# Optimization experiments

Measured on AMD Instinct MI355X. Metric: run time of the kernel, lower is better.

Reference implementation:

```python
import jax, jax.numpy as jnp
import numpy as np

LN_EPS = 1e-5

def setup_inputs() -> dict:
    key = jax.random.key(0)
    ks = jax.random.split(key, 8)
    B, L, D, H = 4, 2048, 512, 8
    x = jax.random.normal(ks[0], (B, L, D), dtype=jnp.float32)
    token_ids = jax.random.randint(ks[1], (B, L), 0, 50000, dtype=jnp.int64)
    s = 1.0 / np.sqrt(D)
    Wq = jax.random.normal(ks[2], (D, D), dtype=jnp.float32) * s
    Wk = jax.random.normal(ks[3], (D, D), dtype=jnp.float32) * s
    Wv = jax.random.normal(ks[4], (D, D), dtype=jnp.float32) * s
    Wo = jax.random.normal(ks[5], (D, D), dtype=jnp.float32) * s
    gamma = jnp.ones((D,), dtype=jnp.float32)
    beta = jnp.zeros((D,), dtype=jnp.float32)
    return {"x": x, "token_ids": token_ids, "Wq": Wq, "Wk": Wk,
            "Wv": Wv, "Wo": Wo, "gamma": gamma, "beta": beta}

def reference(x, token_ids, Wq, Wk, Wv, Wo, gamma, beta):
    B, L, D = x.shape
    H = 8
    Dh = D // H
    residual = x
    # Pre-LN
    mu = jnp.mean(x, axis=-1, keepdims=True)
    var = jnp.mean(jnp.square(x - mu), axis=-1, keepdims=True)
    xn = (x - mu) * jax.lax.rsqrt(var + LN_EPS) * gamma + beta
    # projections (torch Linear: y = x @ W.T), split heads -> [B,H,L,Dh]
    def proj(W):
        return jnp.einsum('bld,ed->ble', xn, W).reshape(B, L, H, Dh).transpose(0, 2, 1, 3)
    Q, K, V = proj(Wq), proj(Wk), proj(Wv)
    scale = jnp.sqrt(jnp.float32(Dh))
    scores = jnp.einsum('bhqd,bhkd->bhqk', Q, K) / scale  # [B,H,L,L]
    neg_inf = jnp.float32(-jnp.inf)
    causal = jnp.triu(jnp.ones((L, L), dtype=bool), k=1)           # [L,L]
    pad = (token_ids == 0)[:, None, None, :]                       # [B,1,1,L]
    scores = jnp.where(causal[None, None], neg_inf, scores)
    scores = jnp.where(pad, neg_inf, scores)
    all_masked = jnp.all(jnp.isinf(scores), axis=-1, keepdims=True)
    scores = jnp.where(all_masked, 0.0, scores)
    attn = jax.nn.softmax(scores, axis=-1)  # dropout is identity in eval
    out = jnp.einsum('bhqk,bhkd->bhqd', attn, V)
    out = out.transpose(0, 2, 1, 3).reshape(B, L, D)
    out = jnp.einsum('bld,ed->ble', out, Wo)
    return residual + out
```

## Files before the change

### kernel.cpp

```cpp
#include <hip/hip_runtime.h>
#include <math.h>

typedef unsigned short u16;
typedef unsigned int u32;
typedef unsigned long long u64;
typedef float f32x4 __attribute__((ext_vector_type(4)));
typedef __bf16 bf16x8 __attribute__((ext_vector_type(8)));
typedef __bf16 bf16x4 __attribute__((ext_vector_type(4)));

constexpr int Bc = 4, Lc = 2048, Dc = 512, Hc = 8, DHc = 64;
constexpr int NTOK = Bc * Lc;
constexpr float LN_EPS = 1e-5f;
constexpr int KS = 72;
constexpr int PS = 72;
constexpr float QSCALE = 0.125f * 1.44269504088896340736f;

__device__ inline u16 bf_bits(float f) {
  return __builtin_bit_cast(u16, (__bf16)f);
}

__global__ __launch_bounds__(256) void cvt4_kernel(const float* __restrict__ s0,
                                                   const float* __restrict__ s1,
                                                   const float* __restrict__ s2,
                                                   const float* __restrict__ s3,
                                                   u16* __restrict__ d0,
                                                   u16* __restrict__ d1,
                                                   u16* __restrict__ d2,
                                                   u16* __restrict__ d3) {
  int mat = blockIdx.x >> 8;
  int i = ((blockIdx.x & 255) * 256 + threadIdx.x) * 4;
  const float* s = (mat == 0) ? s0 : (mat == 1) ? s1 : (mat == 2) ? s2 : s3;
  u16* d = (mat == 0) ? d0 : (mat == 1) ? d1 : (mat == 2) ? d2 : d3;
  float4 v = *(const float4*)&s[i];
  bf16x4 o;
  o[0] = (__bf16)v.x; o[1] = (__bf16)v.y; o[2] = (__bf16)v.z; o[3] = (__bf16)v.w;
  *(bf16x4*)&d[i] = o;
}

__global__ __launch_bounds__(256) void pmask_kernel(const int* __restrict__ tok,
                                                    u64* __restrict__ pm) {
  int wid = (blockIdx.x * 256 + threadIdx.x) >> 6;
  int lane = threadIdx.x & 63;
  u64 m = __ballot(tok[(size_t)wid * 64 + lane] == 0);
  if (lane == 0) pm[wid] = m;
}

__global__ __launch_bounds__(256) void ln_kernel(const float* __restrict__ x,
                                                 const float* __restrict__ gamma,
                                                 const float* __restrict__ beta,
                                                 u16* __restrict__ xn) {
  int wave = threadIdx.x >> 6;
  int lane = threadIdx.x & 63;
  int row  = blockIdx.x * 4 + wave;
  const float* xr = x + (size_t)row * Dc;
  float4 v0 = ((const float4*)xr)[lane * 2];
  float4 v1 = ((const float4*)xr)[lane * 2 + 1];
  float sum = v0.x + v0.y + v0.z + v0.w + v1.x + v1.y + v1.z + v1.w;
  float sq  = v0.x*v0.x + v0.y*v0.y + v0.z*v0.z + v0.w*v0.w
            + v1.x*v1.x + v1.y*v1.y + v1.z*v1.z + v1.w*v1.w;
  #pragma unroll
  for (int off = 32; off > 0; off >>= 1) {
    sum += __shfl_xor(sum, off);
    sq  += __shfl_xor(sq, off);
  }
  float mu = sum * (1.0f / Dc);
  float rs = rsqrtf(sq * (1.0f / Dc) - mu * mu + LN_EPS);
  float4 g0 = ((const float4*)gamma)[lane * 2];
  float4 g1 = ((const float4*)gamma)[lane * 2 + 1];
  float4 b0 = ((const float4*)beta)[lane * 2];
  float4 b1 = ((const float4*)beta)[lane * 2 + 1];
  bf16x8 o;
  o[0] = (__bf16)((v0.x - mu) * rs * g0.x + b0.x);
  o[1] = (__bf16)((v0.y - mu) * rs * g0.y + b0.y);
  o[2] = (__bf16)((v0.z - mu) * rs * g0.z + b0.z);
  o[3] = (__bf16)((v0.w - mu) * rs * g0.w + b0.w);
  o[4] = (__bf16)((v1.x - mu) * rs * g1.x + b1.x);
  o[5] = (__bf16)((v1.y - mu) * rs * g1.y + b1.y);
  o[6] = (__bf16)((v1.z - mu) * rs * g1.z + b1.z);
  o[7] = (__bf16)((v1.w - mu) * rs * g1.w + b1.w);
  *(bf16x8*)&xn[(size_t)row * Dc + lane * 8] = o;
}

template <int MODE>
__global__ __launch_bounds__(256) void gemm_bf16(const u16* __restrict__ A,
                                                 const u16* __restrict__ W,
                                                 const float* __restrict__ res,
                                                 float* __restrict__ out_f,
                                                 u16* __restrict__ o_q,
                                                 u16* __restrict__ o_k,
                                                 u16* __restrict__ o_v,
                                                 float* __restrict__ vm) {
  __shared__ u16 As[128 * KS];
  __shared__ u16 Bs[128 * KS];
  int tid = threadIdx.x;
  int lane = tid & 63;
  int w = tid >> 6;
  int wr = w >> 1, wc = w & 1;
  int cc = lane & 15, rb = lane >> 4;
  int n0 = blockIdx.x * 128;
  int e0 = blockIdx.y * 128;
  f32x4 acc[4][4] = {};
  for (int k0 = 0; k0 < Dc; k0 += 64) {
    #pragma unroll
    for (int u = 0; u < 4; u++) {
      int idx = u * 256 + tid;
      int row = idx >> 3;
      int col = (idx & 7) << 3;
      *(uint4*)&As[row * KS + col] = *(const uint4*)&A[(size_t)(n0 + row) * Dc + k0 + col];
      *(uint4*)&Bs[row * KS + col] = *(const uint4*)&W[(size_t)(e0 + row) * Dc + k0 + col];
    }
    __syncthreads();
    #pragma unroll
    for (int kk = 0; kk < 64; kk += 32) {
      bf16x8 aF[4], bF[4];
      #pragma unroll
      for (int m = 0; m < 4; m++)
        aF[m] = *(bf16x8*)&As[(wr * 64 + m * 16 + cc) * KS + kk + rb * 8];
      #pragma unroll
      for (int n = 0; n < 4; n++)
        bF[n] = *(bf16x8*)&Bs[(wc * 64 + n * 16 + cc) * KS + kk + rb * 8];
      #pragma unroll
      for (int m = 0; m < 4; m++)
        #pragma unroll
        for (int n = 0; n < 4; n++)
          acc[m][n] = __builtin_amdgcn_mfma_f32_16x16x32_bf16(aF[m], bF[n], acc[m][n], 0, 0, 0);
    }
    __syncthreads();
  }
  if (MODE == 3) {
    int bb = n0 >> 11;
    #pragma unroll
    for (int n = 0; n < 4; n++) {
      int c = e0 + wc * 64 + n * 16 + cc;
      int mat = c >> 9;
      int cm = c & 511;
      int h = cm >> 6, dh = cm & 63;
      if (mat == 2) {
        float cp = 0.f;
        #pragma unroll
        for (int m = 0; m < 4; m++) {
          int l0 = (n0 + wr * 64 + m * 16 + rb * 4) & (Lc - 1);
          bf16x4 o4;
          o4[0] = (__bf16)acc[m][n][0]; o4[1] = (__bf16)acc[m][n][1];
          o4[2] = (__bf16)acc[m][n][2]; o4[3] = (__bf16)acc[m][n][3];
          *(bf16x4*)&o_v[((size_t)(bb * Hc + h) * DHc + dh) * Lc + l0] = o4;
          cp += (acc[m][n][0] + acc[m][n][1]) + (acc[m][n][2] + acc[m][n][3]);
        }
        cp += __shfl_xor(cp, 16);
        cp += __shfl_xor(cp, 32);
        if (lane < 16) atomicAdd(&vm[(bb * Hc + h) * DHc + dh], cp);
      } else {
        u16* dst = (mat == 0) ? o_q : o_k;
        float sc = (mat == 0) ? QSCALE : 1.0f;
        #pragma unroll
        for (int m = 0; m < 4; m++) {
          #pragma unroll
          for (int j = 0; j < 4; j++) {
            int r = n0 + wr * 64 + m * 16 + rb * 4 + j;
            int ll = r & (Lc - 1);
            dst[(((size_t)(bb * Hc + h)) * Lc + ll) * DHc + dh] = bf_bits(acc[m][n][j] * sc);
          }
        }
      }
    }
  } else {
    #pragma unroll
    for (int m = 0; m < 4; m++) {
      #pragma unroll
      for (int n = 0; n < 4; n++) {
        #pragma unroll
        for (int j = 0; j < 4; j++) {
          int r = n0 + wr * 64 + m * 16 + rb * 4 + j;
          int c = e0 + wc * 64 + n * 16 + cc;
          size_t o = (size_t)r * Dc + c;
          out_f[o] = acc[m][n][j] + res[o];
        }
      }
    }
  }
}

__global__ __launch_bounds__(64) void attn3(const u16* __restrict__ Q,
                                            const u16* __restrict__ K,
                                            const u16* __restrict__ VT,
                                            const float* __restrict__ vm,
                                            const u64* __restrict__ pmask,
                                            u16* __restrict__ out) {
  __shared__ u16 Ps[32 * PS];
  int lane = threadIdx.x;
  int cc = lane & 15, rb = lane >> 4;
  int bh = blockIdx.x;
  int qt = (int)gridDim.y - 1 - (int)blockIdx.y;
  int q0 = qt * 32;
  int b = bh >> 3, h = bh & 7;
  const u16* Qb = Q + (size_t)bh * Lc * DHc;
  const u16* Kb = K + (size_t)bh * Lc * DHc;
  const u16* Vb = VT + (size_t)bh * DHc * Lc;
  const u64* pmb = pmask + (b << 5);

  bf16x8 qF[2][2];
  #pragma unroll
  for (int qb = 0; qb < 2; qb++)
    #pragma unroll
    for (int kc = 0; kc < 2; kc++)
      qF[qb][kc] = *(const bf16x8*)&Qb[(size_t)(q0 + qb * 16 + cc) * DHc + kc * 32 + rb * 8];

  float mrow[2] = {-INFINITY, -INFINITY};
  float lrow[2] = {0.f, 0.f};
  f32x4 acc[2][4] = {};
  int nfull = q0 >> 6;

  bf16x8 kf[4][2];
  #pragma unroll
  for (int c = 0; c < 4; c++) {
    const u16* kp = &Kb[(size_t)(c * 16 + cc) * DHc + rb * 8];
    kf[c][0] = *(const bf16x8*)kp;
    kf[c][1] = *(const bf16x8*)(kp + 32);
  }

  for (int kt = 0; kt <= nfull; kt++) {
    int k0 = kt * 64;
    bool last = (kt == nfull);
    u64 pm = pmb[kt];
    bf16x8 vf[2][4];
    #pragma unroll
    for (int kc = 0; kc < 2; kc++)
      #pragma unroll
      for (int d0 = 0; d0 < 4; d0++)
        vf[kc][d0] = *(const bf16x8*)&Vb[(size_t)(d0 * 16 + cc) * Lc + k0 + kc * 32 + rb * 8];

    f32x4 sq[2][4] = {};
    __builtin_amdgcn_s_setprio(1);
    #pragma unroll
    for (int c = 0; c < 4; c++) {
      #pragma unroll
      for (int qb = 0; qb < 2; qb++) {
        sq[qb][c] = __builtin_amdgcn_mfma_f32_16x16x32_bf16(kf[c][0], qF[qb][0], sq[qb][c], 0, 0, 0);
        sq[qb][c] = __builtin_amdgcn_mfma_f32_16x16x32_bf16(kf[c][1], qF[qb][1], sq[qb][c], 0, 0, 0);
      }
    }
    __builtin_amdgcn_s_setprio(0);
    if (!last) {
      #pragma unroll
      for (int c = 0; c < 4; c++) {
        const u16* kp = &Kb[(size_t)(k0 + 64 + c * 16 + cc) * DHc + rb * 8];
        kf[c][0] = *(const bf16x8*)kp;
        kf[c][1] = *(const bf16x8*)(kp + 32);
      }
    }
    #pragma unroll
    for (int c = 0; c < 4; c++) {
      u32 smr = (((u32)(pm >> (c * 16)) & 0xffffu) >> (rb * 4));
      #pragma unroll
      for (int qb = 0; qb < 2; qb++)
        #pragma unroll
        for (int j = 0; j < 4; j++)
          if ((smr >> j) & 1) sq[qb][c][j] = -INFINITY;
    }
    if (last) {
      #pragma unroll
      for (int qb = 0; qb < 2; qb++) {
        int qrel = q0 + qb * 16 + cc - k0;
        #pragma unroll
        for (int c = 0; c < 4; c++)
          #pragma unroll
          for (int j = 0; j < 4; j++)
            if (c * 16 + rb * 4 + j > qrel) sq[qb][c][j] = -INFINITY;
      }
    }
    #pragma unroll
    for (int qb = 0; qb < 2; qb++) {
      float m0 = fmaxf(fmaxf(sq[qb][0][0], sq[qb][0][1]), fmaxf(sq[qb][0][2], sq[qb][0][3]));
      float m1 = fmaxf(fmaxf(sq[qb][1][0], sq[qb][1][1]), fmaxf(sq[qb][1][2], sq[qb][1][3]));
      float m2 = fmaxf(fmaxf(sq[qb][2][0], sq[qb][2][1]), fmaxf(sq[qb][2][2], sq[qb][2][3]));
      float m3 = fmaxf(fmaxf(sq[qb][3][0], sq[qb][3][1]), fmaxf(sq[qb][3][2], sq[qb][3][3]));
      float mx = fmaxf(fmaxf(m0, m1), fmaxf(m2, m3));
      mx = fmaxf(mx, __shfl_xor(mx, 16));
      mx = fmaxf(mx, __shfl_xor(mx, 32));
      if (!__all(mx <= mrow[qb] + 8.f)) {
        float nm = fmaxf(mrow[qb], mx);
        float nm2 = fmaxf(nm, -1e30f);
        float alpha = exp2f(mrow[qb] - nm2);
        lrow[qb] *= alpha;
        #pragma unroll
        for (int d0 = 0; d0 < 4; d0++)
          #pragma unroll
          for (int j = 0; j < 4; j++)
            acc[qb][d0][j] *= alpha;
        mrow[qb] = nm;
      }
      float nm2 = fmaxf(mrow[qb], -1e30f);
      float rs = 0.f;
      #pragma unroll
      for (int c = 0; c < 4; c++) {
        f32x4 p;
        #pragma unroll
        for (int j = 0; j < 4; j++) p[j] = exp2f(sq[qb][c][j] - nm2);
        rs += (p[0] + p[1]) + (p[2] + p[3]);
        bf16x4 p4;
        p4[0] = (__bf16)p[0]; p4[1] = (__bf16)p[1];
        p4[2] = (__bf16)p[2]; p4[3] = (__bf16)p[3];
        *(bf16x4*)&Ps[(qb * 16 + cc) * PS + c * 16 + rb * 4] = p4;
      }
      rs += __shfl_xor(rs, 16);
      rs += __shfl_xor(rs, 32);
      lrow[qb] += rs;
    }
    asm volatile("s_waitcnt lgkmcnt(0)" ::: "memory");
    __builtin_amdgcn_sched_barrier(0);
    __builtin_amdgcn_s_setprio(1);
    #pragma unroll
    for (int kc = 0; kc < 2; kc++) {
      bf16x8 pF0 = *(bf16x8*)&Ps[(size_t)cc * PS + kc * 32 + rb * 8];
      bf16x8 pF1 = *(bf16x8*)&Ps[(size_t)(16 + cc) * PS + kc * 32 + rb * 8];
      #pragma unroll
      for (int d0 = 0; d0 < 4; d0++) {
        acc[0][d0] = __builtin_amdgcn_mfma_f32_16x16x32_bf16(vf[kc][d0], pF0, acc[0][d0], 0, 0, 0);
        acc[1][d0] = __builtin_amdgcn_mfma_f32_16x16x32_bf16(vf[kc][d0], pF1, acc[1][d0], 0, 0, 0);
      }
    }
    __builtin_amdgcn_s_setprio(0);
  }
  #pragma unroll
  for (int qb = 0; qb < 2; qb++) {
    int q = q0 + qb * 16 + cc;
    bool ok = lrow[qb] > 0.f;
    float inv = ok ? 1.0f / lrow[qb] : 0.f;
    #pragma unroll
    for (int d0 = 0; d0 < 4; d0++) {
      bf16x4 o4;
      #pragma unroll
      for (int j = 0; j < 4; j++) {
        float v = ok ? acc[qb][d0][j] * inv
                     : vm[bh * DHc + d0 * 16 + rb * 4 + j] * (1.0f / Lc);
        o4[j] = (__bf16)v;
      }
      *(bf16x4*)&out[((size_t)(b * Lc + q)) * Dc + h * DHc + d0 * 16 + rb * 4] = o4;
    }
  }
}

extern "C" void kernel_launch(void* const* d_in, const int* in_sizes, int n_in,
                              void* d_out, int out_size, void* d_ws, size_t ws_size,
                              hipStream_t stream) {
  const float* x     = (const float*)d_in[0];
  const int*   tok   = (const int*)d_in[1];
  const float* Wq    = (const float*)d_in[2];
  const float* Wk    = (const float*)d_in[3];
  const float* Wv    = (const float*)d_in[4];
  const float* Wo    = (const float*)d_in[5];
  const float* gamma = (const float*)d_in[6];
  const float* beta  = (const float*)d_in[7];
  float* out = (float*)d_out;

  const size_t SEG = (size_t)NTOK * Dc;
  const size_t WSEG = (size_t)Dc * Dc;
  u16* xn   = (u16*)d_ws;
  u16* Qd   = xn + SEG;
  u16* Kd   = Qd + SEG;
  u16* VT   = Kd + SEG;
  u16* ao   = VT + SEG;
  u16* Wqkv = ao + SEG;
  u16* Wob  = Wqkv + 3 * WSEG;
  float* vm = (float*)(Wob + WSEG);
  u64* pmarr = (u64*)(vm + (size_t)Bc * Hc * DHc);

  (void)hipMemsetAsync(vm, 0, (size_t)Bc * Hc * DHc * sizeof(float), stream);

  cvt4_kernel<<<1024, 256, 0, stream>>>(Wq, Wk, Wv, Wo,
                                        Wqkv, Wqkv + WSEG, Wqkv + 2 * WSEG, Wob);
  ln_kernel<<<NTOK / 4, 256, 0, stream>>>(x, gamma, beta, xn);
  pmask_kernel<<<32, 256, 0, stream>>>(tok, pmarr);

  dim3 gq(NTOK / 128, (3 * Dc) / 128);
  gemm_bf16<3><<<gq, 256, 0, stream>>>(xn, Wqkv, nullptr, nullptr, Qd, Kd, VT, vm);

  dim3 ga(Bc * Hc, Lc / 32);
  attn3<<<ga, 64, 0, stream>>>(Qd, Kd, VT, vm, pmarr, ao);

  dim3 gg(NTOK / 128, Dc / 128);
  gemm_bf16<0><<<gg, 256, 0, stream>>>(ao, Wob, x, out, nullptr, nullptr, nullptr, nullptr);
}
```

Measured before the change: 123.5 us.

## Split attention KV loop across two waves, stage GEMM epilogues through LDS, retile V

The attention kernel now runs two waves per block, each handling alternate 64-key tiles, and merges their online-softmax states through shared memory at the end. It also skips padding-mask application when a tile holds no padded tokens. V is stored in 64-token tiles so each tile is contiguous, and the QKV and output GEMM epilogues go through LDS so global stores (and residual loads) are coalesced vectors instead of scattered scalars. The weight-convert and pad-mask kernels are fused into one launch. The cost is more LDS use, extra barriers, and a merge step at the end of attention.

After: 135.9 us. +10.1%, slower.

```diff
diff --git a/kernel.cpp b/kernel.cpp
--- a/kernel.cpp
+++ b/kernel.cpp
@@ -19,30 +19,32 @@
   return __builtin_bit_cast(u16, (__bf16)f);
 }
 
-__global__ __launch_bounds__(256) void cvt4_kernel(const float* __restrict__ s0,
+__global__ __launch_bounds__(256) void prep_kernel(const float* __restrict__ s0,
                                                    const float* __restrict__ s1,
                                                    const float* __restrict__ s2,
                                                    const float* __restrict__ s3,
                                                    u16* __restrict__ d0,
                                                    u16* __restrict__ d1,
                                                    u16* __restrict__ d2,
-                                                   u16* __restrict__ d3) {
-  int mat = blockIdx.x >> 8;
-  int i = ((blockIdx.x & 255) * 256 + threadIdx.x) * 4;
-  const float* s = (mat == 0) ? s0 : (mat == 1) ? s1 : (mat == 2) ? s2 : s3;
-  u16* d = (mat == 0) ? d0 : (mat == 1) ? d1 : (mat == 2) ? d2 : d3;
-  float4 v = *(const float4*)&s[i];
-  bf16x4 o;
-  o[0] = (__bf16)v.x; o[1] = (__bf16)v.y; o[2] = (__bf16)v.z; o[3] = (__bf16)v.w;
-  *(bf16x4*)&d[i] = o;
-}
-
-__global__ __launch_bounds__(256) void pmask_kernel(const int* __restrict__ tok,
-                                                    u64* __restrict__ pm) {
-  int wid = (blockIdx.x * 256 + threadIdx.x) >> 6;
-  int lane = threadIdx.x & 63;
-  u64 m = __ballot(tok[(size_t)wid * 64 + lane] == 0);
-  if (lane == 0) pm[wid] = m;
+                                                   u16* __restrict__ d3,
+                                                   const int* __restrict__ tok,
+                                                   u64* __restrict__ pm) {
+  int bid = blockIdx.x;
+  if (bid < 1024) {
+    int mat = bid >> 8;
+    int i = ((bid & 255) * 256 + threadIdx.x) * 4;
+    const float* s = (mat == 0) ? s0 : (mat == 1) ? s1 : (mat == 2) ? s2 : s3;
+    u16* d = (mat == 0) ? d0 : (mat == 1) ? d1 : (mat == 2) ? d2 : d3;
+    float4 v = *(const float4*)&s[i];
+    bf16x4 o;
+    o[0] = (__bf16)v.x; o[1] = (__bf16)v.y; o[2] = (__bf16)v.z; o[3] = (__bf16)v.w;
+    *(bf16x4*)&d[i] = o;
+  } else {
+    int wid = ((bid - 1024) * 256 + threadIdx.x) >> 6;
+    int lane = threadIdx.x & 63;
+    u64 m = __ballot(tok[(size_t)wid * 64 + lane] == 0);
+    if (lane == 0) pm[wid] = m;
+  }
 }
 
 __global__ __launch_bounds__(256) void ln_kernel(const float* __restrict__ x,
@@ -90,8 +92,9 @@
                                                  u16* __restrict__ o_k,
                                                  u16* __restrict__ o_v,
                                                  float* __restrict__ vm) {
-  __shared__ u16 As[128 * KS];
-  __shared__ u16 Bs[128 * KS];
+  __shared__ u16 lds[2 * 128 * KS];
+  u16* As = lds;
+  u16* Bs = lds + 128 * KS;
   int tid = threadIdx.x;
   int lane = tid & 63;
   int w = tid >> 6;
@@ -129,65 +132,94 @@
   }
   if (MODE == 3) {
     int bb = n0 >> 11;
-    #pragma unroll
-    for (int n = 0; n < 4; n++) {
-      int c = e0 + wc * 64 + n * 16 + cc;
-      int mat = c >> 9;
-      int cm = c & 511;
-      int h = cm >> 6, dh = cm & 63;
-      if (mat == 2) {
+    int mat = e0 >> 9;
+    int e0c = e0 & 511;
+    if (mat == 2) {
+      #pragma unroll
+      for (int n = 0; n < 4; n++) {
+        int c = e0c + wc * 64 + n * 16 + cc;
+        int h = c >> 6, dh = c & 63;
         float cp = 0.f;
         #pragma unroll
         for (int m = 0; m < 4; m++) {
-          int l0 = (n0 + wr * 64 + m * 16 + rb * 4) & (Lc - 1);
+          int l = (n0 + wr * 64 + m * 16 + rb * 4) & (Lc - 1);
           bf16x4 o4;
           o4[0] = (__bf16)acc[m][n][0]; o4[1] = (__bf16)acc[m][n][1];
           o4[2] = (__bf16)acc[m][n][2]; o4[3] = (__bf16)acc[m][n][3];
-          *(bf16x4*)&o_v[((size_t)(bb * Hc + h) * DHc + dh) * Lc + l0] = o4;
+          size_t addr = ((((size_t)(bb * Hc + h)) * (Lc / 64) + (l >> 6)) * DHc + dh) * 64 + (l & 63);
+          *(bf16x4*)&o_v[addr] = o4;
           cp += (acc[m][n][0] + acc[m][n][1]) + (acc[m][n][2] + acc[m][n][3]);
         }
         cp += __shfl_xor(cp, 16);
         cp += __shfl_xor(cp, 32);
         if (lane < 16) atomicAdd(&vm[(bb * Hc + h) * DHc + dh], cp);
-      } else {
-        u16* dst = (mat == 0) ? o_q : o_k;
-        float sc = (mat == 0) ? QSCALE : 1.0f;
-        #pragma unroll
-        for (int m = 0; m < 4; m++) {
+      }
+    } else {
+      float sc = (mat == 0) ? QSCALE : 1.0f;
+      u16* dst0 = (mat == 0) ? o_q : o_k;
+      const int TS = 136;
+      u16* Ts = lds;
+      int wbase = (wr * 64 + rb * 4) * TS + wc * 64 + cc;
+      #pragma unroll
+      for (int m = 0; m < 4; m++)
+        #pragma unroll
+        for (int n = 0; n < 4; n++)
           #pragma unroll
-          for (int j = 0; j < 4; j++) {
-            int r = n0 + wr * 64 + m * 16 + rb * 4 + j;
-            int ll = r & (Lc - 1);
-            dst[(((size_t)(bb * Hc + h)) * Lc + ll) * DHc + dh] = bf_bits(acc[m][n][j] * sc);
-          }
-        }
-      }
+          for (int j = 0; j < 4; j++)
+            Ts[wbase + (m * 16 + j) * TS + n * 16] = bf_bits(acc[m][n][j] * sc);
+      __syncthreads();
+      int r = tid >> 1, ch = (tid & 1) << 6;
+      int nn = n0 + r;
+      int l = nn & (Lc - 1);
+      int h = (e0c + ch) >> 6;
+      u16* dp = dst0 + (((size_t)(bb * Hc + h)) * Lc + l) * DHc;
+      #pragma unroll
+      for (int u = 0; u < 8; u++)
+        *(bf16x8*)&dp[u * 8] = *(bf16x8*)&Ts[r * TS + ch + u * 8];
     }
   } else {
-    #pragma unroll
-    for (int m = 0; m < 4; m++) {
-      #pragma unroll
-      for (int n = 0; n < 4; n++) {
-        #pragma unroll
-        for (int j = 0; j < 4; j++) {
-          int r = n0 + wr * 64 + m * 16 + rb * 4 + j;
-          int c = e0 + wc * 64 + n * 16 + cc;
-          size_t o = (size_t)r * Dc + c;
-          out_f[o] = acc[m][n][j] + res[o];
-        }
-      }
-    }
-  }
-}
-
-__global__ __launch_bounds__(64) void attn3(const u16* __restrict__ Q,
-                                            const u16* __restrict__ K,
-                                            const u16* __restrict__ VT,
-                                            const float* __restrict__ vm,
-                                            const u64* __restrict__ pmask,
-                                            u16* __restrict__ out) {
-  __shared__ u16 Ps[32 * PS];
-  int lane = threadIdx.x;
+    const int TF = 129;
+    float* Tf = (float*)lds;
+    #pragma unroll
+    for (int hp = 0; hp < 2; hp++) {
+      __syncthreads();
+      if (wr == hp) {
+        #pragma unroll
+        for (int m = 0; m < 4; m++)
+          #pragma unroll
+          for (int n = 0; n < 4; n++)
+            #pragma unroll
+            for (int j = 0; j < 4; j++)
+              Tf[(m * 16 + rb * 4 + j) * TF + wc * 64 + n * 16 + cc] = acc[m][n][j];
+      }
+      __syncthreads();
+      int r = tid >> 2, cq = (tid & 3) << 5;
+      size_t off = (size_t)(n0 + hp * 64 + r) * Dc + e0 + cq;
+      #pragma unroll
+      for (int u = 0; u < 8; u++) {
+        float4 rv = *(const float4*)&res[off + u * 4];
+        float4 tv = *(float4*)&Tf[r * TF + cq + u * 4];
+        float4 ov;
+        ov.x = rv.x + tv.x; ov.y = rv.y + tv.y;
+        ov.z = rv.z + tv.z; ov.w = rv.w + tv.w;
+        *(float4*)&out_f[off + u * 4] = ov;
+      }
+    }
+  }
+}
+
+__global__ __launch_bounds__(128) void attn4(const u16* __restrict__ Q,
+                                             const u16* __restrict__ K,
+                                             const u16* __restrict__ VT,
+                                             const float* __restrict__ vm,
+                                             const u64* __restrict__ pmask,
+                                             u16* __restrict__ out) {
+  __shared__ u16 Ps[2][32 * PS];
+  __shared__ float Msh[2][64], Lsh[2][64];
+  __shared__ float Accs[2][4][256];
+  int tid = threadIdx.x;
+  int w = tid >> 6;
+  int lane = tid & 63;
   int cc = lane & 15, rb = lane >> 4;
   int bh = blockIdx.x;
   int qt = (int)gridDim.y - 1 - (int)blockIdx.y;
@@ -195,7 +227,7 @@
   int b = bh >> 3, h = bh & 7;
   const u16* Qb = Q + (size_t)bh * Lc * DHc;
   const u16* Kb = K + (size_t)bh * Lc * DHc;
-  const u16* Vb = VT + (size_t)bh * DHc * Lc;
+  const u16* Vb = VT + (size_t)bh * Lc * DHc;
   const u64* pmb = pmask + (b << 5);
 
   bf16x8 qF[2][2];
@@ -211,23 +243,26 @@
   int nfull = q0 >> 6;
 
   bf16x8 kf[4][2];
-  #pragma unroll
-  for (int c = 0; c < 4; c++) {
-    const u16* kp = &Kb[(size_t)(c * 16 + cc) * DHc + rb * 8];
-    kf[c][0] = *(const bf16x8*)kp;
-    kf[c][1] = *(const bf16x8*)(kp + 32);
-  }
-
-  for (int kt = 0; kt <= nfull; kt++) {
+  if (w <= nfull) {
+    const u16* kp0 = Kb + (size_t)(w * 64) * DHc;
+    #pragma unroll
+    for (int c = 0; c < 4; c++) {
+      kf[c][0] = *(const bf16x8*)&kp0[(c * 16 + cc) * DHc + rb * 8];
+      kf[c][1] = *(const bf16x8*)&kp0[(c * 16 + cc) * DHc + 32 + rb * 8];
+    }
+  }
+
+  for (int kt = w; kt <= nfull; kt += 2) {
     int k0 = kt * 64;
     bool last = (kt == nfull);
     u64 pm = pmb[kt];
+    const u16* vp = Vb + (size_t)kt * (DHc * 64);
     bf16x8 vf[2][4];
     #pragma unroll
     for (int kc = 0; kc < 2; kc++)
       #pragma unroll
       for (int d0 = 0; d0 < 4; d0++)
-        vf[kc][d0] = *(const bf16x8*)&Vb[(size_t)(d0 * 16 + cc) * Lc + k0 + kc * 32 + rb * 8];
+        vf[kc][d0] = *(const bf16x8*)&vp[(d0 * 16 + cc) * 64 + kc * 32 + rb * 8];
 
     f32x4 sq[2][4] = {};
     __builtin_amdgcn_s_setprio(1);
@@ -240,22 +275,24 @@
       }
     }
     __builtin_amdgcn_s_setprio(0);
-    if (!last) {
+    if (kt + 2 <= nfull) {
+      const u16* kp = Kb + (size_t)(k0 + 128) * DHc;
       #pragma unroll
       for (int c = 0; c < 4; c++) {
-        const u16* kp = &Kb[(size_t)(k0 + 64 + c * 16 + cc) * DHc + rb * 8];
-        kf[c][0] = *(const bf16x8*)kp;
-        kf[c][1] = *(const bf16x8*)(kp + 32);
-      }
-    }
-    #pragma unroll
-    for (int c = 0; c < 4; c++) {
-      u32 smr = (((u32)(pm >> (c * 16)) & 0xffffu) >> (rb * 4));
-      #pragma unroll
-      for (int qb = 0; qb < 2; qb++)
-        #pragma unroll
-        for (int j = 0; j < 4; j++)
-          if ((smr >> j) & 1) sq[qb][c][j] = -INFINITY;
+        kf[c][0] = *(const bf16x8*)&kp[(c * 16 + cc) * DHc + rb * 8];
+        kf[c][1] = *(const bf16x8*)&kp[(c * 16 + cc) * DHc + 32 + rb * 8];
+      }
+    }
+    if (pm) {
+      #pragma unroll
+      for (int c = 0; c < 4; c++) {
+        u32 smr = (((u32)(pm >> (c * 16)) & 0xffffu) >> (rb * 4));
+        #pragma unroll
+        for (int qb = 0; qb < 2; qb++)
+          #pragma unroll
+          for (int j = 0; j < 4; j++)
+            if ((smr >> j) & 1) sq[qb][c][j] = -INFINITY;
+      }
     }
     if (last) {
       #pragma unroll
@@ -300,7 +337,7 @@
         bf16x4 p4;
         p4[0] = (__bf16)p[0]; p4[1] = (__bf16)p[1];
         p4[2] = (__bf16)p[2]; p4[3] = (__bf16)p[3];
-        *(bf16x4*)&Ps[(qb * 16 + cc) * PS + c * 16 + rb * 4] = p4;
+        *(bf16x4*)&Ps[w][(qb * 16 + cc) * PS + c * 16 + rb * 4] = p4;
       }
       rs += __shfl_xor(rs, 16);
       rs += __shfl_xor(rs, 32);
@@ -311,8 +348,8 @@
     __builtin_amdgcn_s_setprio(1);
     #pragma unroll
     for (int kc = 0; kc < 2; kc++) {
-      bf16x8 pF0 = *(bf16x8*)&Ps[(size_t)cc * PS + kc * 32 + rb * 8];
-      bf16x8 pF1 = *(bf16x8*)&Ps[(size_t)(16 + cc) * PS + kc * 32 + rb * 8];
+      bf16x8 pF0 = *(bf16x8*)&Ps[w][(size_t)cc * PS + kc * 32 + rb * 8];
+      bf16x8 pF1 = *(bf16x8*)&Ps[w][(size_t)(16 + cc) * PS + kc * 32 + rb * 8];
       #pragma unroll
       for (int d0 = 0; d0 < 4; d0++) {
         acc[0][d0] = __builtin_amdgcn_mfma_f32_16x16x32_bf16(vf[kc][d0], pF0, acc[0][d0], 0, 0, 0);
@@ -321,21 +358,51 @@
     }
     __builtin_amdgcn_s_setprio(0);
   }
-  #pragma unroll
-  for (int qb = 0; qb < 2; qb++) {
-    int q = q0 + qb * 16 + cc;
-    bool ok = lrow[qb] > 0.f;
-    float inv = ok ? 1.0f / lrow[qb] : 0.f;
-    #pragma unroll
-    for (int d0 = 0; d0 < 4; d0++) {
-      bf16x4 o4;
-      #pragma unroll
-      for (int j = 0; j < 4; j++) {
-        float v = ok ? acc[qb][d0][j] * inv
-                     : vm[bh * DHc + d0 * 16 + rb * 4 + j] * (1.0f / Lc);
-        o4[j] = (__bf16)v;
-      }
-      *(bf16x4*)&out[((size_t)(b * Lc + q)) * Dc + h * DHc + d0 * 16 + rb * 4] = o4;
+
+  if (w == 1) {
+    #pragma unroll
+    for (int qb = 0; qb < 2; qb++) {
+      Msh[qb][lane] = mrow[qb];
+      Lsh[qb][lane] = lrow[qb];
+      #pragma unroll
+      for (int d0 = 0; d0 < 4; d0++)
+        *(f32x4*)&Accs[qb][d0][lane * 4] = acc[qb][d0];
+    }
+  }
+  __syncthreads();
+  if (w == 0) {
+    #pragma unroll
+    for (int qb = 0; qb < 2; qb++) {
+      float m1 = Msh[qb][lane], l1 = Lsh[qb][lane];
+      float ms = fmaxf(mrow[qb], m1);
+      float msc = fmaxf(ms, -1e30f);
+      float a0 = exp2f(mrow[qb] - msc);
+      float a1 = exp2f(m1 - msc);
+      lrow[qb] = lrow[qb] * a0 + l1 * a1;
+      #pragma unroll
+      for (int d0 = 0; d0 < 4; d0++) {
+        f32x4 o1 = *(f32x4*)&Accs[qb][d0][lane * 4];
+        #pragma unroll
+        for (int j = 0; j < 4; j++)
+          acc[qb][d0][j] = acc[qb][d0][j] * a0 + o1[j] * a1;
+      }
+    }
+    #pragma unroll
+    for (int qb = 0; qb < 2; qb++) {
+      int q = q0 + qb * 16 + cc;
+      bool ok = lrow[qb] > 0.f;
+      float inv = ok ? 1.0f / lrow[qb] : 0.f;
+      #pragma unroll
+      for (int d0 = 0; d0 < 4; d0++) {
+        bf16x4 o4;
+        #pragma unroll
+        for (int j = 0; j < 4; j++) {
+          float v = ok ? acc[qb][d0][j] * inv
+                       : vm[bh * DHc + d0 * 16 + rb * 4 + j] * (1.0f / Lc);
+          o4[j] = (__bf16)v;
+        }
+        *(bf16x4*)&out[((size_t)(b * Lc + q)) * Dc + h * DHc + d0 * 16 + rb * 4] = o4;
+      }
     }
   }
 }
@@ -367,16 +434,16 @@
 
   (void)hipMemsetAsync(vm, 0, (size_t)Bc * Hc * DHc * sizeof(float), stream);
 
-  cvt4_kernel<<<1024, 256, 0, stream>>>(Wq, Wk, Wv, Wo,
-                                        Wqkv, Wqkv + WSEG, Wqkv + 2 * WSEG, Wob);
+  prep_kernel<<<1056, 256, 0, stream>>>(Wq, Wk, Wv, Wo,
+                                        Wqkv, Wqkv + WSEG, Wqkv + 2 * WSEG, Wob,
+                                        tok, pmarr);
   ln_kernel<<<NTOK / 4, 256, 0, stream>>>(x, gamma, beta, xn);
-  pmask_kernel<<<32, 256, 0, stream>>>(tok, pmarr);
 
   dim3 gq(NTOK / 128, (3 * Dc) / 128);
   gemm_bf16<3><<<gq, 256, 0, stream>>>(xn, Wqkv, nullptr, nullptr, Qd, Kd, VT, vm);
 
   dim3 ga(Bc * Hc, Lc / 32);
-  attn3<<<ga, 64, 0, stream>>>(Qd, Kd, VT, vm, pmarr, ao);
+  attn4<<<ga, 128, 0, stream>>>(Qd, Kd, VT, vm, pmarr, ao);
 
   dim3 gg(NTOK / 128, Dc / 128);
   gemm_bf16<0><<<gg, 256, 0, stream>>>(ao, Wob, x, out, nullptr, nullptr, nullptr, nullptr);
```

## Tile V layout per 64-key block, double-buffer K prefetch, merge prep kernels

Applied to the files above, without the earlier changes.

Stores V transposed in 64-key tiles so each attention iteration reads a contiguous 8KB block instead of strided rows. K fragments are double-buffered two tiles ahead through a lambda body unrolled by two, giving loads more time to land. The weight-convert and pad-mask kernels are merged into one launch, the padding mask is skipped when the tile has no pads, and the QKV epilogue is branched per block on which matrix it writes. These changes add register pressure from the second K buffer, and the finite -1e30 initial max changes the edge handling for fully masked rows.

Result: faster. 120.2 us (-2.7%).

```diff
diff --git a/kernel.cpp b/kernel.cpp
--- a/kernel.cpp
+++ b/kernel.cpp
@@ -14,35 +14,38 @@
 constexpr int KS = 72;
 constexpr int PS = 72;
 constexpr float QSCALE = 0.125f * 1.44269504088896340736f;
+constexpr float MNEG = -1e30f;
 
 __device__ inline u16 bf_bits(float f) {
   return __builtin_bit_cast(u16, (__bf16)f);
 }
 
-__global__ __launch_bounds__(256) void cvt4_kernel(const float* __restrict__ s0,
+__global__ __launch_bounds__(256) void prep_kernel(const float* __restrict__ s0,
                                                    const float* __restrict__ s1,
                                                    const float* __restrict__ s2,
                                                    const float* __restrict__ s3,
                                                    u16* __restrict__ d0,
                                                    u16* __restrict__ d1,
                                                    u16* __restrict__ d2,
-                                                   u16* __restrict__ d3) {
-  int mat = blockIdx.x >> 8;
-  int i = ((blockIdx.x & 255) * 256 + threadIdx.x) * 4;
-  const float* s = (mat == 0) ? s0 : (mat == 1) ? s1 : (mat == 2) ? s2 : s3;
-  u16* d = (mat == 0) ? d0 : (mat == 1) ? d1 : (mat == 2) ? d2 : d3;
-  float4 v = *(const float4*)&s[i];
-  bf16x4 o;
-  o[0] = (__bf16)v.x; o[1] = (__bf16)v.y; o[2] = (__bf16)v.z; o[3] = (__bf16)v.w;
-  *(bf16x4*)&d[i] = o;
-}
-
-__global__ __launch_bounds__(256) void pmask_kernel(const int* __restrict__ tok,
-                                                    u64* __restrict__ pm) {
-  int wid = (blockIdx.x * 256 + threadIdx.x) >> 6;
-  int lane = threadIdx.x & 63;
-  u64 m = __ballot(tok[(size_t)wid * 64 + lane] == 0);
-  if (lane == 0) pm[wid] = m;
+                                                   u16* __restrict__ d3,
+                                                   const int* __restrict__ tok,
+                                                   u64* __restrict__ pm) {
+  int bid = blockIdx.x;
+  if (bid < 1024) {
+    int mat = bid >> 8;
+    int i = ((bid & 255) * 256 + threadIdx.x) * 4;
+    const float* s = (mat == 0) ? s0 : (mat == 1) ? s1 : (mat == 2) ? s2 : s3;
+    u16* d = (mat == 0) ? d0 : (mat == 1) ? d1 : (mat == 2) ? d2 : d3;
+    float4 v = *(const float4*)&s[i];
+    bf16x4 o;
+    o[0] = (__bf16)v.x; o[1] = (__bf16)v.y; o[2] = (__bf16)v.z; o[3] = (__bf16)v.w;
+    *(bf16x4*)&d[i] = o;
+  } else {
+    int wid = ((bid - 1024) * 256 + threadIdx.x) >> 6;
+    int lane = threadIdx.x & 63;
+    u64 m = __ballot(tok[(size_t)wid * 64 + lane] == 0);
+    if (lane == 0) pm[wid] = m;
+  }
 }
 
 __global__ __launch_bounds__(256) void ln_kernel(const float* __restrict__ x,
@@ -129,36 +132,41 @@
   }
   if (MODE == 3) {
     int bb = n0 >> 11;
-    #pragma unroll
-    for (int n = 0; n < 4; n++) {
-      int c = e0 + wc * 64 + n * 16 + cc;
-      int mat = c >> 9;
-      int cm = c & 511;
-      int h = cm >> 6, dh = cm & 63;
-      if (mat == 2) {
+    int mat = e0 >> 9;
+    int e0c = e0 & 511;
+    if (mat == 2) {
+      #pragma unroll
+      for (int n = 0; n < 4; n++) {
+        int c = e0c + wc * 64 + n * 16 + cc;
+        int h = c >> 6, dh = c & 63;
         float cp = 0.f;
         #pragma unroll
         for (int m = 0; m < 4; m++) {
-          int l0 = (n0 + wr * 64 + m * 16 + rb * 4) & (Lc - 1);
+          int l = (n0 + wr * 64 + m * 16 + rb * 4) & (Lc - 1);
           bf16x4 o4;
           o4[0] = (__bf16)acc[m][n][0]; o4[1] = (__bf16)acc[m][n][1];
           o4[2] = (__bf16)acc[m][n][2]; o4[3] = (__bf16)acc[m][n][3];
-          *(bf16x4*)&o_v[((size_t)(bb * Hc + h) * DHc + dh) * Lc + l0] = o4;
+          size_t addr = ((((size_t)(bb * Hc + h)) * (Lc / 64) + (l >> 6)) * DHc + dh) * 64 + (l & 63);
+          *(bf16x4*)&o_v[addr] = o4;
           cp += (acc[m][n][0] + acc[m][n][1]) + (acc[m][n][2] + acc[m][n][3]);
         }
         cp += __shfl_xor(cp, 16);
         cp += __shfl_xor(cp, 32);
         if (lane < 16) atomicAdd(&vm[(bb * Hc + h) * DHc + dh], cp);
-      } else {
-        u16* dst = (mat == 0) ? o_q : o_k;
-        float sc = (mat == 0) ? QSCALE : 1.0f;
-        #pragma unroll
-        for (int m = 0; m < 4; m++) {
+      }
+    } else {
+      float sc = (mat == 0) ? QSCALE : 1.0f;
+      u16* dst = (mat == 0) ? o_q : o_k;
+      #pragma unroll
+      for (int m = 0; m < 4; m++) {
+        #pragma unroll
+        for (int n = 0; n < 4; n++) {
           #pragma unroll
           for (int j = 0; j < 4; j++) {
             int r = n0 + wr * 64 + m * 16 + rb * 4 + j;
+            int c = e0c + wc * 64 + n * 16 + cc;
             int ll = r & (Lc - 1);
-            dst[(((size_t)(bb * Hc + h)) * Lc + ll) * DHc + dh] = bf_bits(acc[m][n][j] * sc);
+            dst[(((size_t)(bb * Hc + (c >> 6))) * Lc + ll) * DHc + (c & 63)] = bf_bits(acc[m][n][j] * sc);
           }
         }
       }
@@ -180,12 +188,12 @@
   }
 }
 
-__global__ __launch_bounds__(64) void attn3(const u16* __restrict__ Q,
-                                            const u16* __restrict__ K,
-                                            const u16* __restrict__ VT,
-                                            const float* __restrict__ vm,
-                                            const u64* __restrict__ pmask,
-                                            u16* __restrict__ out) {
+__global__ __launch_bounds__(64) void attn11(const u16* __restrict__ Q,
+                                             const u16* __restrict__ K,
+                                             const u16* __restrict__ VT,
+                                             const float* __restrict__ vm,
+                                             const u64* __restrict__ pmask,
+                                             u16* __restrict__ out) {
   __shared__ u16 Ps[32 * PS];
   int lane = threadIdx.x;
   int cc = lane & 15, rb = lane >> 4;
@@ -195,8 +203,9 @@
   int b = bh >> 3, h = bh & 7;
   const u16* Qb = Q + (size_t)bh * Lc * DHc;
   const u16* Kb = K + (size_t)bh * Lc * DHc;
-  const u16* Vb = VT + (size_t)bh * DHc * Lc;
+  const u16* Vb = VT + (size_t)bh * Lc * DHc;
   const u64* pmb = pmask + (b << 5);
+  int nfull = q0 >> 6;
 
   bf16x8 qF[2][2];
   #pragma unroll
@@ -205,29 +214,39 @@
     for (int kc = 0; kc < 2; kc++)
       qF[qb][kc] = *(const bf16x8*)&Qb[(size_t)(q0 + qb * 16 + cc) * DHc + kc * 32 + rb * 8];
 
-  float mrow[2] = {-INFINITY, -INFINITY};
+  float mrow[2] = {MNEG, MNEG};
   float lrow[2] = {0.f, 0.f};
   f32x4 acc[2][4] = {};
-  int nfull = q0 >> 6;
-
-  bf16x8 kf[4][2];
-  #pragma unroll
-  for (int c = 0; c < 4; c++) {
-    const u16* kp = &Kb[(size_t)(c * 16 + cc) * DHc + rb * 8];
-    kf[c][0] = *(const bf16x8*)kp;
-    kf[c][1] = *(const bf16x8*)(kp + 32);
-  }
-
-  for (int kt = 0; kt <= nfull; kt++) {
+
+  bf16x8 kfA[4][2], kfB[4][2];
+  {
+    const u16* kp = Kb;
+    #pragma unroll
+    for (int c = 0; c < 4; c++) {
+      kfA[c][0] = *(const bf16x8*)&kp[(c * 16 + cc) * DHc + rb * 8];
+      kfA[c][1] = *(const bf16x8*)&kp[(c * 16 + cc) * DHc + 32 + rb * 8];
+    }
+  }
+  if (nfull >= 1) {
+    const u16* kp = Kb + (size_t)64 * DHc;
+    #pragma unroll
+    for (int c = 0; c < 4; c++) {
+      kfB[c][0] = *(const bf16x8*)&kp[(c * 16 + cc) * DHc + rb * 8];
+      kfB[c][1] = *(const bf16x8*)&kp[(c * 16 + cc) * DHc + 32 + rb * 8];
+    }
+  }
+
+  auto body = [&](int kt, bf16x8 (&kf)[4][2]) {
     int k0 = kt * 64;
     bool last = (kt == nfull);
     u64 pm = pmb[kt];
+    const u16* vp = Vb + (size_t)kt * (DHc * 64);
     bf16x8 vf[2][4];
     #pragma unroll
     for (int kc = 0; kc < 2; kc++)
       #pragma unroll
       for (int d0 = 0; d0 < 4; d0++)
-        vf[kc][d0] = *(const bf16x8*)&Vb[(size_t)(d0 * 16 + cc) * Lc + k0 + kc * 32 + rb * 8];
+        vf[kc][d0] = *(const bf16x8*)&vp[(d0 * 16 + cc) * 64 + kc * 32 + rb * 8];
 
     f32x4 sq[2][4] = {};
     __builtin_amdgcn_s_setprio(1);
@@ -240,22 +259,24 @@
       }
     }
     __builtin_amdgcn_s_setprio(0);
-    if (!last) {
+    if (kt + 2 <= nfull) {
+      const u16* kp = Kb + (size_t)(k0 + 128) * DHc;
       #pragma unroll
       for (int c = 0; c < 4; c++) {
-        const u16* kp = &Kb[(size_t)(k0 + 64 + c * 16 + cc) * DHc + rb * 8];
-        kf[c][0] = *(const bf16x8*)kp;
-        kf[c][1] = *(const bf16x8*)(kp + 32);
-      }
-    }
-    #pragma unroll
-    for (int c = 0; c < 4; c++) {
-      u32 smr = (((u32)(pm >> (c * 16)) & 0xffffu) >> (rb * 4));
-      #pragma unroll
-      for (int qb = 0; qb < 2; qb++)
-        #pragma unroll
-        for (int j = 0; j < 4; j++)
-          if ((smr >> j) & 1) sq[qb][c][j] = -INFINITY;
+        kf[c][0] = *(const bf16x8*)&kp[(c * 16 + cc) * DHc + rb * 8];
+        kf[c][1] = *(const bf16x8*)&kp[(c * 16 + cc) * DHc + 32 + rb * 8];
+      }
+    }
+    if (pm) {
+      #pragma unroll
+      for (int c = 0; c < 4; c++) {
+        u32 smr = (((u32)(pm >> (c * 16)) & 0xffffu) >> (rb * 4));
+        #pragma unroll
+        for (int qb = 0; qb < 2; qb++)
+          #pragma unroll
+          for (int j = 0; j < 4; j++)
+            if ((smr >> j) & 1) sq[qb][c][j] = -INFINITY;
+      }
     }
     if (last) {
       #pragma unroll
@@ -279,8 +300,7 @@
       mx = fmaxf(mx, __shfl_xor(mx, 32));
       if (!__all(mx <= mrow[qb] + 8.f)) {
         float nm = fmaxf(mrow[qb], mx);
-        float nm2 = fmaxf(nm, -1e30f);
-        float alpha = exp2f(mrow[qb] - nm2);
+        float alpha = exp2f(mrow[qb] - nm);
         lrow[qb] *= alpha;
         #pragma unroll
         for (int d0 = 0; d0 < 4; d0++)
@@ -289,13 +309,12 @@
             acc[qb][d0][j] *= alpha;
         mrow[qb] = nm;
       }
-      float nm2 = fmaxf(mrow[qb], -1e30f);
       float rs = 0.f;
       #pragma unroll
       for (int c = 0; c < 4; c++) {
         f32x4 p;
         #pragma unroll
-        for (int j = 0; j < 4; j++) p[j] = exp2f(sq[qb][c][j] - nm2);
+        for (int j = 0; j < 4; j++) p[j] = exp2f(sq[qb][c][j] - mrow[qb]);
         rs += (p[0] + p[1]) + (p[2] + p[3]);
         bf16x4 p4;
         p4[0] = (__bf16)p[0]; p4[1] = (__bf16)p[1];
@@ -320,7 +339,13 @@
       }
     }
     __builtin_amdgcn_s_setprio(0);
-  }
+  };
+
+  for (int kt = 0; kt <= nfull; kt += 2) {
+    body(kt, kfA);
+    if (kt + 1 <= nfull) body(kt + 1, kfB);
+  }
+
   #pragma unroll
   for (int qb = 0; qb < 2; qb++) {
     int q = q0 + qb * 16 + cc;
@@ -367,16 +392,16 @@
 
   (void)hipMemsetAsync(vm, 0, (size_t)Bc * Hc * DHc * sizeof(float), stream);
 
-  cvt4_kernel<<<1024, 256, 0, stream>>>(Wq, Wk, Wv, Wo,
-                                        Wqkv, Wqkv + WSEG, Wqkv + 2 * WSEG, Wob);
+  prep_kernel<<<1056, 256, 0, stream>>>(Wq, Wk, Wv, Wo,
+                                        Wqkv, Wqkv + WSEG, Wqkv + 2 * WSEG, Wob,
+                                        tok, pmarr);
   ln_kernel<<<NTOK / 4, 256, 0, stream>>>(x, gamma, beta, xn);
-  pmask_kernel<<<32, 256, 0, stream>>>(tok, pmarr);
 
   dim3 gq(NTOK / 128, (3 * Dc) / 128);
   gemm_bf16<3><<<gq, 256, 0, stream>>>(xn, Wqkv, nullptr, nullptr, Qd, Kd, VT, vm);
 
   dim3 ga(Bc * Hc, Lc / 32);
-  attn3<<<ga, 64, 0, stream>>>(Qd, Kd, VT, vm, pmarr, ao);
+  attn11<<<ga, 64, 0, stream>>>(Qd, Kd, VT, vm, pmarr, ao);
 
   dim3 gg(NTOK / 128, Dc / 128);
   gemm_bf16<0><<<gg, 256, 0, stream>>>(ao, Wob, x, out, nullptr, nullptr, nullptr, nullptr);
```
